# Kernel tuning notes

Hardware: AMD Instinct MI355X
Metric: run time of the kernel (lower is better)

## Reference

```python
import jax, jax.numpy as jnp
import numpy as np
from jax import lax

BN_EPS = 1e-5


def _spatial_gate(x, w, g, b, m, v):
    # x: [N, C, H, W]; ChannelPool -> [N, 2, H, W]; 7x7 conv -> [N,1,H,W]; BN (eval); sigmoid gate
    comp = jnp.stack([jnp.max(x, axis=1), jnp.mean(x, axis=1)], axis=1)
    o = lax.conv_general_dilated(comp, w, (1, 1), [(3, 3), (3, 3)],
                                 dimension_numbers=('NCHW', 'OIHW', 'NCHW'))
    o = (o - m[None, :, None, None]) * lax.rsqrt(v + BN_EPS)[None, :, None, None] \
        * g[None, :, None, None] + b[None, :, None, None]
    s = jax.nn.sigmoid(o)
    return x * s


def _eca_sort(x, w_eca):
    # global avg pool -> sort channels desc -> 1D conv over sorted seq -> sigmoid -> unsort -> gate
    y = jnp.mean(x, axis=(2, 3))               # [N, C]
    order = jnp.argsort(-y, axis=1)            # descending sort indices
    rank = jnp.argsort(order, axis=1)          # inverse permutation
    ys = jnp.take_along_axis(y, order, axis=1)  # sorted descending
    k = w_eca.shape[-1]
    p = k // 2
    o = lax.conv_general_dilated(ys[:, None, :], w_eca, (1,), [(p, p)],
                                 dimension_numbers=('NCH', 'OIH', 'NCH'))[:, 0, :]
    sig = jax.nn.sigmoid(o)
    yr = jnp.take_along_axis(sig, rank, axis=1)  # reorder back per original index_select(rank)
    return x * yr[:, :, None, None]


def setup_inputs() -> dict:
    key = jax.random.key(0)
    ks = jax.random.split(key, 6)
    N, C, H, W = 32, 256, 56, 56
    inp = {
        'x': jax.random.normal(ks[0], (N, C, H, W), dtype=jnp.float32),
        'weight': jax.random.normal(ks[1], (1,), dtype=jnp.float32),
        'w_h': jax.random.normal(ks[2], (1, 2, 7, 7), dtype=jnp.float32) * 0.1,
        'g_h': jnp.ones((1,), jnp.float32), 'b_h': jnp.zeros((1,), jnp.float32),
        'm_h': jnp.zeros((1,), jnp.float32), 'v_h': jnp.ones((1,), jnp.float32),
        'w_w': jax.random.normal(ks[3], (1, 2, 7, 7), dtype=jnp.float32) * 0.1,
        'g_w': jnp.ones((1,), jnp.float32), 'b_w': jnp.zeros((1,), jnp.float32),
        'm_w': jnp.zeros((1,), jnp.float32), 'v_w': jnp.ones((1,), jnp.float32),
        'w_s': jax.random.normal(ks[4], (1, 2, 7, 7), dtype=jnp.float32) * 0.1,
        'g_s': jnp.ones((1,), jnp.float32), 'b_s': jnp.zeros((1,), jnp.float32),
        'm_s': jnp.zeros((1,), jnp.float32), 'v_s': jnp.ones((1,), jnp.float32),
        'w_eca': jax.random.normal(ks[5], (1, 1, 5), dtype=jnp.float32) * 0.3,
    }
    return inp


def reference(x, weight, w_h, g_h, b_h, m_h, v_h, w_w, g_w, b_w, m_w, v_w,
              w_s, g_s, b_s, m_s, v_s, w_eca):
    # branch 1: gate over H-as-channel (permute 0,2,1,3)
    xh = jnp.transpose(x, (0, 2, 1, 3))
    x11 = jnp.transpose(_spatial_gate(xh, w_h, g_h, b_h, m_h, v_h), (0, 2, 1, 3))
    # branch 2: gate over W-as-channel (permute 0,3,2,1)
    xw = jnp.transpose(x, (0, 3, 2, 1))
    x21 = jnp.transpose(_spatial_gate(xw, w_w, g_w, b_w, m_w, v_w), (0, 3, 2, 1))
    # branch 3: eca with sort/unsort
    x31 = _eca_sort(x, w_eca)
    # branch 4: plain spatial gate
    xo = _spatial_gate(x, w_s, g_s, b_s, m_s, v_s)
    return 0.23779 * xo + 0.24695 * x11 + 0.24365 * x21 + 0.27173 * x31
```

## Files before the change

kernel.cpp:

```cpp
#include <hip/hip_runtime.h>
#include <math.h>

#define N_ 32
#define C_ 256
#define H_ 56
#define W_ 56
#define HW_ (H_*W_)
#define HW4_ (HW_/4)
#define CHW_ (C_*HW_)
#define NHW_ (N_*HW_)
#define NHW4_ (NHW_/4)
#define NCW_ (N_*C_*W_)
#define NHC_ (N_*H_*C_)
#define BN_EPS_ 1e-5f

#define PPW 8
#define NB_PL 1024

#define F4MAX(a,b) do { (a).x=fmaxf((a).x,(b).x); (a).y=fmaxf((a).y,(b).y); \
                        (a).z=fmaxf((a).z,(b).z); (a).w=fmaxf((a).w,(b).w); } while(0)
#define F4ADD(a,b) do { (a).x+=(b).x; (a).y+=(b).y; (a).z+=(b).z; (a).w+=(b).w; } while(0)

__global__ __launch_bounds__(64) void pools_k(
        const float* __restrict__ x,
        float* __restrict__ maxH, float* __restrict__ meanH,
        float* __restrict__ maxWt, float* __restrict__ meanWt,
        float* __restrict__ pmx, float* __restrict__ psm,
        float* __restrict__ y) {
    __shared__ float2 rowscr[56 * 15];
    __shared__ float4 colmx[56];
    __shared__ float4 colsm[56];
    const int wid = blockIdx.x;
    const int lane = threadIdx.x;
    const int n = wid >> 5;
    const int pb0 = wid * PPW;
    const float4* x4 = (const float4*)x;
    const int lc = (lane < 56) ? lane : 55;
    const int g = lane / 14;
    const int q = lane - g * 14;

    float4 A[14], B[14];
    float4 amx[14], asum[14];
    #pragma unroll
    for (int t = 0; t < 14; ++t) {
        amx[t] = make_float4(-INFINITY, -INFINITY, -INFINITY, -INFINITY);
        asum[t] = make_float4(0.f, 0.f, 0.f, 0.f);
    }

#define ISSUE(S, P) do { size_t _ba = (size_t)(pb0 + (P)) * HW4_;                  \
        _Pragma("unroll")                                                          \
        for (int _t = 0; _t < 14; ++_t) S[_t] = x4[_ba + 56 * _t + lc]; } while(0)

#define PLANE(S, K) do {                                                           \
        const int _pb = pb0 + (K);                                                 \
        const int _c = _pb & 255;                                                  \
        float4 cmx = S[0], csm = S[0];                                             \
        _Pragma("unroll")                                                          \
        for (int t = 1; t < 14; ++t) { F4MAX(cmx, S[t]); F4ADD(csm, S[t]); }       \
        _Pragma("unroll")                                                          \
        for (int t = 0; t < 14; ++t) { F4MAX(amx[t], S[t]); F4ADD(asum[t], S[t]); }\
        if (lane < 56) {                                                           \
            _Pragma("unroll")                                                      \
            for (int t = 0; t < 14; ++t) {                                         \
                float hm = fmaxf(fmaxf(S[t].x, S[t].y), fmaxf(S[t].z, S[t].w));    \
                float hs = S[t].x + S[t].y + S[t].z + S[t].w;                      \
                rowscr[(4 * t + g) * 15 + q] = make_float2(hm, hs);                \
            }                                                                      \
            colmx[g * 14 + q] = cmx;                                               \
            colsm[g * 14 + q] = csm;                                               \
        }                                                                          \
        if ((K) + 2 < PPW) ISSUE(S, (K) + 2);         \
        if (lane < 56) {                               \
            float rmx = -INFINITY, rsm = 0.f;                                      \
            _Pragma("unroll")                                                      \
            for (int j = 0; j < 14; ++j) {                                         \
                float2 p = rowscr[lane * 15 + j];                                  \
                rmx = fmaxf(rmx, p.x); rsm += p.y;                                 \
            }                                                                      \
            int o = (n * C_ + _c) * H_ + lane;          \
            maxWt[o] = rmx; meanWt[o] = rsm * (1.f / W_);                          \
        }                                                                          \
        float ysum = 0.f;                                                          \
        if (lane < 14) {                        \
            float4 gm = colmx[lane], gs = colsm[lane];                             \
            _Pragma("unroll")                                                      \
            for (int j = 1; j < 4; ++j) {                                          \
                F4MAX(gm, colmx[j * 14 + lane]);                                   \
                F4ADD(gs, colsm[j * 14 + lane]);                                   \
            }                                                                      \
            ((float4*)maxH)[(n * C_ + _c) * 14 + lane] = gm;                       \
            float4 mh = make_float4(gs.x * (1.f / H_), gs.y * (1.f / H_),          \
                                    gs.z * (1.f / H_), gs.w * (1.f / H_));         \
            ((float4*)meanH)[(n * C_ + _c) * 14 + lane] = mh;                      \
            ysum = gs.x + gs.y + gs.z + gs.w;                                      \
        }                                                                          \
        ysum += __shfl_down(ysum, 8); ysum += __shfl_down(ysum, 4);                \
        ysum += __shfl_down(ysum, 2); ysum += __shfl_down(ysum, 1);                \
        if (lane == 0) y[_pb] = ysum * (1.f / HW_);                                \
    } while(0)

    ISSUE(A, 0);
    ISSUE(B, 1);
    #pragma unroll
    for (int k2 = 0; k2 < PPW / 2; ++k2) {
        PLANE(A, 2 * k2);
        PLANE(B, 2 * k2 + 1);
    }
#undef ISSUE
#undef PLANE
    if (lane < 56) {
        float4* PM = (float4*)pmx + (size_t)wid * HW4_;
        float4* PS = (float4*)psm + (size_t)wid * HW4_;
        #pragma unroll
        for (int t = 0; t < 14; ++t) {
            PM[56 * t + lane] = amx[t];
            PS[56 * t + lane] = asum[t];
        }
    }
}

__global__ __launch_bounds__(256, 4) void cpool_final_k(
        const float* __restrict__ pmx, const float* __restrict__ psm,
        float* __restrict__ maxC, float* __restrict__ meanC) {
    __shared__ float4 smx[4][64];
    __shared__ float4 ssm[4][64];
    int bb = blockIdx.x;
    int tid = threadIdx.x;
    int oi = tid & 63, g4 = tid >> 6;
    int t = bb * 64 + oi;
    int n = t / HW4_, hw4 = t - n * HW4_;
    const float4* PM = (const float4*)pmx + (size_t)(n * 32 + g4 * 8) * HW4_ + hw4;
    const float4* PS = (const float4*)psm + (size_t)(n * 32 + g4 * 8) * HW4_ + hw4;
    float4 mx = make_float4(-INFINITY, -INFINITY, -INFINITY, -INFINITY);
    float4 sm = make_float4(0.f, 0.f, 0.f, 0.f);
    #pragma unroll
    for (int g = 0; g < 8; ++g) {
        float4 v = PM[(size_t)g * HW4_];
        float4 s = PS[(size_t)g * HW4_];
        F4MAX(mx, v);
        F4ADD(sm, s);
    }
    smx[g4][oi] = mx;
    ssm[g4][oi] = sm;
    __syncthreads();
    if (tid < 64) {
        float4 m = smx[0][tid];
        #pragma unroll
        for (int j = 1; j < 4; ++j) F4MAX(m, smx[j][tid]);
        ((float4*)maxC)[bb * 64 + tid] = m;
    } else if (tid < 128) {
        int t2 = tid - 64;
        float4 s = ssm[0][t2];
        #pragma unroll
        for (int j = 1; j < 4; ++j) F4ADD(s, ssm[j][t2]);
        s.x *= (1.f / C_); s.y *= (1.f / C_); s.z *= (1.f / C_); s.w *= (1.f / C_);
        ((float4*)meanC)[bb * 64 + t2] = s;
    }
}

template <int R, int Cc, bool TR>
__device__ __forceinline__ void conv7_part(int t, const float* __restrict__ p0,
                                           const float* __restrict__ p1,
                                           const float* __restrict__ wt,
                                           float g, float bb, float m, float v,
                                           float* __restrict__ out) {
    const int per = R * Cc;
    int n = t / per;
    int r2 = t - n * per;
    int i = r2 / Cc, j = r2 - i * Cc;
    const float* b0 = p0 + (size_t)n * per;
    const float* b1 = p1 + (size_t)n * per;
    float acc = 0.f;
    #pragma unroll
    for (int ki = 0; ki < 7; ++ki) {
        int ii = i + ki - 3;
        if (ii < 0 || ii >= R) continue;
        #pragma unroll
        for (int kj = 0; kj < 7; ++kj) {
            int jj = j + kj - 3;
            if (jj < 0 || jj >= Cc) continue;
            int idx = ii * Cc + jj;
            int wi = TR ? (kj * 7 + ki) : (ki * 7 + kj);
            acc += b0[idx] * wt[wi] + b1[idx] * wt[49 + wi];
        }
    }
    float o = (acc - m) * rsqrtf(v + BN_EPS_) * g + bb;
    out[t] = 1.f / (1.f + expf(-o));
}

#define NB_SS (NHW_ / 256)
#define NB_SH (NCW_ / 256)
#define NB_SW (NHC_ / 256)

__global__ __launch_bounds__(256) void conv_eca_k(
        const float* __restrict__ maxC, const float* __restrict__ meanC,
        const float* __restrict__ maxH, const float* __restrict__ meanH,
        const float* __restrict__ maxWt, const float* __restrict__ meanWt,
        const float* __restrict__ w_s, const float* __restrict__ g_s,
        const float* __restrict__ b_s, const float* __restrict__ m_s,
        const float* __restrict__ v_s,
        const float* __restrict__ w_h, const float* __restrict__ g_h,
        const float* __restrict__ b_h, const float* __restrict__ m_h,
        const float* __restrict__ v_h,
        const float* __restrict__ w_w, const float* __restrict__ g_w,
        const float* __restrict__ b_w, const float* __restrict__ m_w,
        const float* __restrict__ v_w,
        const float* __restrict__ y, const float* __restrict__ w_eca,
        float* __restrict__ s_s, float* __restrict__ s_h, float* __restrict__ s_wt,
        float* __restrict__ gate) {
    __shared__ float sv[C_];
    __shared__ int si[C_];
    int b = blockIdx.x;
    int tid = threadIdx.x;
    if (b < NB_SS) {
        conv7_part<H_, W_, false>(b * 256 + tid, maxC, meanC, w_s, g_s[0], b_s[0],
                                  m_s[0], v_s[0], s_s);
    } else if (b < NB_SS + NB_SH) {
        conv7_part<C_, W_, false>((b - NB_SS) * 256 + tid, maxH, meanH, w_h, g_h[0],
                                  b_h[0], m_h[0], v_h[0], s_h);
    } else if (b < NB_SS + NB_SH + NB_SW) {
        conv7_part<C_, H_, true>((b - NB_SS - NB_SH) * 256 + tid, maxWt, meanWt, w_w,
                                 g_w[0], b_w[0], m_w[0], v_w[0], s_wt);
    } else {
        int n = b - (NB_SS + NB_SH + NB_SW);
        sv[tid] = y[n * C_ + tid];
        si[tid] = tid;
        __syncthreads();
        for (int k = 2; k <= C_; k <<= 1) {
            for (int j = k >> 1; j > 0; j >>= 1) {
                int ixj = tid ^ j;
                if (ixj > tid) {
                    float v1 = sv[tid], v2 = sv[ixj];
                    int i1 = si[tid], i2 = si[ixj];
                    bool before = (v1 > v2) || (v1 == v2 && i1 < i2);
                    bool dir = ((tid & k) == 0);
                    if (dir ? !before : before) {
                        sv[tid] = v2; sv[ixj] = v1;
                        si[tid] = i2; si[ixj] = i1;
                    }
                }
                __syncthreads();
            }
        }
        float o = 0.f;
        #pragma unroll
        for (int j = 0; j < 5; ++j) {
            int p = tid + j - 2;
            if (p >= 0 && p < C_) o += sv[p] * w_eca[j];
        }
        gate[n * C_ + si[tid]] = 1.f / (1.f + expf(-o));
    }
}

__global__ __launch_bounds__(256) void apply_k(
        const float* __restrict__ x, const float* __restrict__ s_s,
        const float* __restrict__ s_h, const float* __restrict__ s_wt,
        const float* __restrict__ gate, float* __restrict__ out) {
    int t0 = blockIdx.x * 512 + threadIdx.x;
    #pragma unroll
    for (int r = 0; r < 2; ++r) {
        int t = t0 + r * 256;
        int f = t * 4;
        int n = f / CHW_;
        int rem = f - n * CHW_;
        int c = rem / HW_;
        int hw = rem - c * HW_;
        int h = hw / W_;
        int w = hw - h * W_;
        float4 xv = ((const float4*)x)[t];
        float4 s4 = *(const float4*)(s_s + (size_t)n * HW_ + hw);
        float4 h4 = *(const float4*)(s_h + ((size_t)n * C_ + c) * W_ + w);
        float sw = s_wt[((size_t)n * C_ + c) * H_ + h];
        float ge = gate[n * C_ + c];
        float base = 0.24365f * sw + 0.27173f * ge;
        float4 o;
        o.x = xv.x * (0.23779f * s4.x + 0.24695f * h4.x + base);
        o.y = xv.y * (0.23779f * s4.y + 0.24695f * h4.y + base);
        o.z = xv.z * (0.23779f * s4.z + 0.24695f * h4.z + base);
        o.w = xv.w * (0.23779f * s4.w + 0.24695f * h4.w + base);
        ((float4*)out)[t] = o;
    }
}

extern "C" void kernel_launch(void* const* d_in, const int* in_sizes, int n_in,
                              void* d_out, int out_size, void* d_ws, size_t ws_size,
                              hipStream_t stream) {
    const float* x     = (const float*)d_in[0];
    const float* w_h   = (const float*)d_in[2];
    const float* g_h   = (const float*)d_in[3];
    const float* b_h   = (const float*)d_in[4];
    const float* m_h   = (const float*)d_in[5];
    const float* v_h   = (const float*)d_in[6];
    const float* w_w   = (const float*)d_in[7];
    const float* g_w   = (const float*)d_in[8];
    const float* b_w   = (const float*)d_in[9];
    const float* m_w   = (const float*)d_in[10];
    const float* v_w   = (const float*)d_in[11];
    const float* w_s   = (const float*)d_in[12];
    const float* g_s   = (const float*)d_in[13];
    const float* b_s   = (const float*)d_in[14];
    const float* m_s   = (const float*)d_in[15];
    const float* v_s   = (const float*)d_in[16];
    const float* w_eca = (const float*)d_in[17];
    float* out = (float*)d_out;

    float* ws    = (float*)d_ws;
    float* maxC  = ws;
    float* meanC = maxC  + NHW_;
    float* maxH  = meanC + NHW_;
    float* meanH = maxH  + NCW_;
    float* maxWt = meanH + NCW_;
    float* meanWt= maxWt + NHC_;
    float* s_s   = meanWt+ NHC_;
    float* s_h   = s_s   + NHW_;
    float* s_wt  = s_h   + NCW_;
    float* yv    = s_wt  + NHC_;
    float* gate  = yv    + N_ * C_;
    float* pmx   = gate  + N_ * C_;
    float* psm   = pmx   + (size_t)NB_PL * HW_;

    pools_k<<<NB_PL, 64, 0, stream>>>(x, maxH, meanH, maxWt, meanWt, pmx, psm, yv);

    cpool_final_k<<<NHW4_ / 64, 256, 0, stream>>>(pmx, psm, maxC, meanC);

    int conv_blocks = NB_SS + NB_SH + NB_SW + N_;
    conv_eca_k<<<conv_blocks, 256, 0, stream>>>(maxC, meanC, maxH, meanH, maxWt, meanWt,
                                                w_s, g_s, b_s, m_s, v_s,
                                                w_h, g_h, b_h, m_h, v_h,
                                                w_w, g_w, b_w, m_w, v_w,
                                                yv, w_eca, s_s, s_h, s_wt, gate);

    apply_k<<<(N_ * CHW_ / 4) / 512, 256, 0, stream>>>(x, s_s, s_h, s_wt, gate, out);
}
```

Before: 94.65 us.

## Split pooling into per-plane tile kernel and direct channel-pool kernel

Replaces the fused multi-plane pooling kernel, and its partial channel-pool buffers, with two kernels. One computes H/W/global pools per plane through an LDS tile; the other computes the channel max/mean by reading x directly. This removes the write and readback of the partial-sum buffers and the register-heavy pipelined kernel. The cost is reading the input tensor twice, relying on cache to absorb the second pass.

```diff
diff --git a/kernel.cpp b/kernel.cpp
--- a/kernel.cpp
+++ b/kernel.cpp
@@ -8,153 +8,113 @@
 #define HW_ (H_*W_)
 #define HW4_ (HW_/4)
 #define CHW_ (C_*HW_)
+#define CHW4_ (CHW_/4)
 #define NHW_ (N_*HW_)
 #define NHW4_ (NHW_/4)
 #define NCW_ (N_*C_*W_)
 #define NHC_ (N_*H_*C_)
 #define BN_EPS_ 1e-5f
 
-#define PPW 8
-#define NB_PL 1024
+#define TLD 57
 
 #define F4MAX(a,b) do { (a).x=fmaxf((a).x,(b).x); (a).y=fmaxf((a).y,(b).y); \
                         (a).z=fmaxf((a).z,(b).z); (a).w=fmaxf((a).w,(b).w); } while(0)
 #define F4ADD(a,b) do { (a).x+=(b).x; (a).y+=(b).y; (a).z+=(b).z; (a).w+=(b).w; } while(0)
 
-__global__ __launch_bounds__(64) void pools_k(
+__global__ __launch_bounds__(64) void plane_k(
         const float* __restrict__ x,
         float* __restrict__ maxH, float* __restrict__ meanH,
         float* __restrict__ maxWt, float* __restrict__ meanWt,
-        float* __restrict__ pmx, float* __restrict__ psm,
         float* __restrict__ y) {
-    __shared__ float2 rowscr[56 * 15];
-    __shared__ float4 colmx[56];
-    __shared__ float4 colsm[56];
+    __shared__ float tile[H_ * TLD];
     const int wid = blockIdx.x;
     const int lane = threadIdx.x;
-    const int n = wid >> 5;
-    const int pb0 = wid * PPW;
-    const float4* x4 = (const float4*)x;
-    const int lc = (lane < 56) ? lane : 55;
-    const int g = lane / 14;
-    const int q = lane - g * 14;
-
-    float4 A[14], B[14];
-    float4 amx[14], asum[14];
-    #pragma unroll
-    for (int t = 0; t < 14; ++t) {
-        amx[t] = make_float4(-INFINITY, -INFINITY, -INFINITY, -INFINITY);
-        asum[t] = make_float4(0.f, 0.f, 0.f, 0.f);
-    }
-
-#define ISSUE(S, P) do { size_t _ba = (size_t)(pb0 + (P)) * HW4_;                  \
-        _Pragma("unroll")                                                          \
-        for (int _t = 0; _t < 14; ++_t) S[_t] = x4[_ba + 56 * _t + lc]; } while(0)
-
-#define PLANE(S, K) do {                                                           \
-        const int _pb = pb0 + (K);                                                 \
-        const int _c = _pb & 255;                                                  \
-        float4 cmx = S[0], csm = S[0];                                             \
-        _Pragma("unroll")                                                          \
-        for (int t = 1; t < 14; ++t) { F4MAX(cmx, S[t]); F4ADD(csm, S[t]); }       \
-        _Pragma("unroll")                                                          \
-        for (int t = 0; t < 14; ++t) { F4MAX(amx[t], S[t]); F4ADD(asum[t], S[t]); }\
-        if (lane < 56) {                                                           \
-            _Pragma("unroll")                                                      \
-            for (int t = 0; t < 14; ++t) {                                         \
-                float hm = fmaxf(fmaxf(S[t].x, S[t].y), fmaxf(S[t].z, S[t].w));    \
-                float hs = S[t].x + S[t].y + S[t].z + S[t].w;                      \
-                rowscr[(4 * t + g) * 15 + q] = make_float2(hm, hs);                \
-            }                                                                      \
-            colmx[g * 14 + q] = cmx;                                               \
-            colsm[g * 14 + q] = csm;                                               \
-        }                                                                          \
-        if ((K) + 2 < PPW) ISSUE(S, (K) + 2);         \
-        if (lane < 56) {                               \
-            float rmx = -INFINITY, rsm = 0.f;                                      \
-            _Pragma("unroll")                                                      \
-            for (int j = 0; j < 14; ++j) {                                         \
-                float2 p = rowscr[lane * 15 + j];                                  \
-                rmx = fmaxf(rmx, p.x); rsm += p.y;                                 \
-            }                                                                      \
-            int o = (n * C_ + _c) * H_ + lane;          \
-            maxWt[o] = rmx; meanWt[o] = rsm * (1.f / W_);                          \
-        }                                                                          \
-        float ysum = 0.f;                                                          \
-        if (lane < 14) {                        \
-            float4 gm = colmx[lane], gs = colsm[lane];                             \
-            _Pragma("unroll")                                                      \
-            for (int j = 1; j < 4; ++j) {                                          \
-                F4MAX(gm, colmx[j * 14 + lane]);                                   \
-                F4ADD(gs, colsm[j * 14 + lane]);                                   \
-            }                                                                      \
-            ((float4*)maxH)[(n * C_ + _c) * 14 + lane] = gm;                       \
-            float4 mh = make_float4(gs.x * (1.f / H_), gs.y * (1.f / H_),          \
-                                    gs.z * (1.f / H_), gs.w * (1.f / H_));         \
-            ((float4*)meanH)[(n * C_ + _c) * 14 + lane] = mh;                      \
-            ysum = gs.x + gs.y + gs.z + gs.w;                                      \
-        }                                                                          \
-        ysum += __shfl_down(ysum, 8); ysum += __shfl_down(ysum, 4);                \
-        ysum += __shfl_down(ysum, 2); ysum += __shfl_down(ysum, 1);                \
-        if (lane == 0) y[_pb] = ysum * (1.f / HW_);                                \
-    } while(0)
-
-    ISSUE(A, 0);
-    ISSUE(B, 1);
-    #pragma unroll
-    for (int k2 = 0; k2 < PPW / 2; ++k2) {
-        PLANE(A, 2 * k2);
-        PLANE(B, 2 * k2 + 1);
-    }
-#undef ISSUE
-#undef PLANE
-    if (lane < 56) {
-        float4* PM = (float4*)pmx + (size_t)wid * HW4_;
-        float4* PS = (float4*)psm + (size_t)wid * HW4_;
-        #pragma unroll
-        for (int t = 0; t < 14; ++t) {
-            PM[56 * t + lane] = amx[t];
-            PS[56 * t + lane] = asum[t];
-        }
-    }
-}
-
-__global__ __launch_bounds__(256, 4) void cpool_final_k(
-        const float* __restrict__ pmx, const float* __restrict__ psm,
+    const int n = wid >> 8, c = wid & 255;
+    const float4* x4 = (const float4*)x + (size_t)wid * HW4_;
+
+    float4 r[12], rl;
+    #pragma unroll
+    for (int i = 0; i < 12; ++i) r[i] = x4[i * 64 + lane];
+    if (lane < 16) rl = x4[768 + lane];
+    #pragma unroll
+    for (int i = 0; i < 12; ++i) {
+        int u = i * 64 + lane;
+        int row = u / 14, c0 = (u - row * 14) * 4;
+        float* d = &tile[row * TLD + c0];
+        d[0] = r[i].x; d[1] = r[i].y; d[2] = r[i].z; d[3] = r[i].w;
+    }
+    if (lane < 16) {
+        int u = 768 + lane;
+        int row = u / 14, c0 = (u - row * 14) * 4;
+        float* d = &tile[row * TLD + c0];
+        d[0] = rl.x; d[1] = rl.y; d[2] = rl.z; d[3] = rl.w;
+    }
+    float csm = 0.f;
+    if (lane < W_) {
+        float cmx = -INFINITY;
+        #pragma unroll 8
+        for (int j = 0; j < H_; ++j) {
+            float v = tile[j * TLD + lane];
+            cmx = fmaxf(cmx, v); csm += v;
+        }
+        int o = (n * C_ + c) * W_ + lane;
+        maxH[o] = cmx;
+        meanH[o] = csm * (1.f / H_);
+    }
+    float ysum = (lane < W_) ? csm : 0.f;
+    #pragma unroll
+    for (int off = 32; off >= 1; off >>= 1) ysum += __shfl_xor(ysum, off);
+    if (lane == 0) y[n * C_ + c] = ysum * (1.f / HW_);
+    if (lane < H_) {
+        const float* rp = &tile[lane * TLD];
+        float rmx = -INFINITY, rsm = 0.f;
+        #pragma unroll 8
+        for (int j = 0; j < W_; ++j) {
+            float v = rp[j];
+            rmx = fmaxf(rmx, v); rsm += v;
+        }
+        int o = (n * C_ + c) * H_ + lane;
+        maxWt[o] = rmx;
+        meanWt[o] = rsm * (1.f / W_);
+    }
+}
+
+__global__ __launch_bounds__(256) void cpool_k(
+        const float* __restrict__ x,
         float* __restrict__ maxC, float* __restrict__ meanC) {
-    __shared__ float4 smx[4][64];
-    __shared__ float4 ssm[4][64];
+    __shared__ float4 smx[256];
+    __shared__ float4 ssm[256];
     int bb = blockIdx.x;
     int tid = threadIdx.x;
-    int oi = tid & 63, g4 = tid >> 6;
-    int t = bb * 64 + oi;
-    int n = t / HW4_, hw4 = t - n * HW4_;
-    const float4* PM = (const float4*)pmx + (size_t)(n * 32 + g4 * 8) * HW4_ + hw4;
-    const float4* PS = (const float4*)psm + (size_t)(n * 32 + g4 * 8) * HW4_ + hw4;
+    int g = tid >> 5, qi = tid & 31;
+    int q = bb * 32 + qi;
+    int n = q / HW4_;
+    int hw4 = q - n * HW4_;
+    const float4* x4 = (const float4*)x;
+    size_t base = (size_t)n * CHW4_ + hw4 + (size_t)(g * 32) * HW4_;
     float4 mx = make_float4(-INFINITY, -INFINITY, -INFINITY, -INFINITY);
     float4 sm = make_float4(0.f, 0.f, 0.f, 0.f);
-    #pragma unroll
-    for (int g = 0; g < 8; ++g) {
-        float4 v = PM[(size_t)g * HW4_];
-        float4 s = PS[(size_t)g * HW4_];
+    #pragma unroll 16
+    for (int i = 0; i < 32; ++i) {
+        float4 v = x4[base + (size_t)i * HW4_];
         F4MAX(mx, v);
-        F4ADD(sm, s);
-    }
-    smx[g4][oi] = mx;
-    ssm[g4][oi] = sm;
+        F4ADD(sm, v);
+    }
+    smx[g * 32 + qi] = mx;
+    ssm[g * 32 + qi] = sm;
     __syncthreads();
-    if (tid < 64) {
-        float4 m = smx[0][tid];
-        #pragma unroll
-        for (int j = 1; j < 4; ++j) F4MAX(m, smx[j][tid]);
-        ((float4*)maxC)[bb * 64 + tid] = m;
-    } else if (tid < 128) {
-        int t2 = tid - 64;
-        float4 s = ssm[0][t2];
-        #pragma unroll
-        for (int j = 1; j < 4; ++j) F4ADD(s, ssm[j][t2]);
+    if (tid < 32) {
+        float4 m = smx[tid];
+        #pragma unroll
+        for (int j = 1; j < 8; ++j) F4MAX(m, smx[j * 32 + tid]);
+        ((float4*)maxC)[bb * 32 + tid] = m;
+    } else if (tid < 64) {
+        int t2 = tid - 32;
+        float4 s = ssm[t2];
+        #pragma unroll
+        for (int j = 1; j < 8; ++j) F4ADD(s, ssm[j * 32 + t2]);
         s.x *= (1.f / C_); s.y *= (1.f / C_); s.z *= (1.f / C_); s.w *= (1.f / C_);
-        ((float4*)meanC)[bb * 64 + t2] = s;
+        ((float4*)meanC)[bb * 32 + t2] = s;
     }
 }
 
@@ -316,12 +276,10 @@
     float* s_wt  = s_h   + NCW_;
     float* yv    = s_wt  + NHC_;
     float* gate  = yv    + N_ * C_;
-    float* pmx   = gate  + N_ * C_;
-    float* psm   = pmx   + (size_t)NB_PL * HW_;
-
-    pools_k<<<NB_PL, 64, 0, stream>>>(x, maxH, meanH, maxWt, meanWt, pmx, psm, yv);
-
-    cpool_final_k<<<NHW4_ / 64, 256, 0, stream>>>(pmx, psm, maxC, meanC);
+
+    plane_k<<<N_ * C_, 64, 0, stream>>>(x, maxH, meanH, maxWt, meanWt, yv);
+
+    cpool_k<<<NHW4_ / 32, 256, 0, stream>>>(x, maxC, meanC);
 
     int conv_blocks = NB_SS + NB_SH + NB_SW + N_;
     conv_eca_k<<<conv_blocks, 256, 0, stream>>>(maxC, meanC, maxH, meanH, maxWt, meanWt,
```

Result: slower. 100.5 us (+6.1%).
